# Performance work log

Measured on AMD Instinct MI355X. Metric: run time of the kernel, lower is better.

## Reference

```python
import jax, jax.numpy as jnp
import numpy as np


def setup_inputs() -> dict:
    key = jax.random.key(0)
    k1, k2, k3 = jax.random.split(key, 3)
    # q: [num_seqs, num_heads, head_dim] decode queries (q_len = 1)
    q = jax.random.normal(k1, (32, 32, 128), dtype=jnp.float32)
    # k, v: [sp_shards, num_seqs, kv_len_per_shard, num_kv_heads, head_dim]
    k = jax.random.normal(k2, (4, 32, 1024, 8, 128), dtype=jnp.float32)
    v = jax.random.normal(k3, (4, 32, 1024, 8, 128), dtype=jnp.float32)
    return {"q": q, "k": k, "v": v}


def reference(q, k, v):
    # Flash-decoding style paged decode attention with GQA:
    # each sequence-parallel shard s produces a partial (normalized) output
    # plus per-(seq, head) max logit and exp-sum; gatherlayer then performs
    # the online-softmax merge across shards.
    n, h, d = q.shape
    s, _, L, kv, _ = k.shape
    g = h // kv  # GQA group size
    scale = jnp.asarray(d, q.dtype) ** -0.5
    q4 = q.reshape(n, kv, g, d)

    # --- per-shard partial attention (what self.attn returns per rank) ---
    scores = jnp.einsum('nkgd,snlkd->snkgl', q4, k) * scale  # [s,n,kv,g,L]
    max_logits = scores.max(axis=-1)                          # [s,n,kv,g]
    p = jnp.exp(scores - max_logits[..., None])
    exp_sum = p.sum(axis=-1)                                  # [s,n,kv,g]
    partial = jnp.einsum('snkgl,snlkd->snkgd', p, v) / exp_sum[..., None]

    # --- gatherlayer: online-softmax combine across shards ---
    gmax = max_logits.max(axis=0)                             # [n,kv,g]
    w = jnp.exp(max_logits - gmax) * exp_sum                  # [s,n,kv,g]
    out = (partial * w[..., None]).sum(axis=0) / w.sum(axis=0)[..., None]
    return out.reshape(n, h, d)
```

## Files before the change

kernel.cpp:

```cpp
#include <hip/hip_runtime.h>
#include <math.h>

#define NSEQ 32
#define NH   32
#define NKV  8
#define GRP  4
#define DIM  128
#define NSH  4
#define LSH  1024
#define ITERS 128
#define KVSTRIDE (NKV*DIM)

#define MOFF ((size_t)NSH*NSEQ*NKV*GRP*DIM)
#define SOFF (MOFF + (size_t)NSH*NSEQ*NKV*GRP)

__global__ __launch_bounds__(256, 4) void attn_partial_kernel(
    const float* __restrict__ q, const float* __restrict__ kk,
    const float* __restrict__ vv, float* __restrict__ ws) {
  const int kvh = blockIdx.x;
  const int n   = blockIdx.y;
  const int sh  = blockIdx.z;
  const int tid = threadIdx.x;
  const int w    = tid >> 6;
  const int lane = tid & 63;
  const int sub  = lane & 31;
  const int pgrp = (w << 1) | (lane >> 5);

  const float scale = 0.08838834764831845f;
  const float* qp = q + ((size_t)n * NH + (size_t)kvh * GRP) * DIM + sub * 4;
  float4 qv0 = *(const float4*)(qp + 0 * DIM);
  float4 qv1 = *(const float4*)(qp + 1 * DIM);
  float4 qv2 = *(const float4*)(qp + 2 * DIM);
  float4 qv3 = *(const float4*)(qp + 3 * DIM);
#define SCQ(Q) Q.x *= scale; Q.y *= scale; Q.z *= scale; Q.w *= scale
  SCQ(qv0); SCQ(qv1); SCQ(qv2); SCQ(qv3);
#undef SCQ

  float m0 = -1e30f, m1 = -1e30f, m2 = -1e30f, m3 = -1e30f;
  float s0 = 0.f, s1 = 0.f, s2 = 0.f, s3 = 0.f;
  float4 a0 = make_float4(0.f,0.f,0.f,0.f);
  float4 a1 = a0, a2 = a0, a3 = a0;

  const size_t blkoff = ((size_t)sh * NSEQ + n) * LSH * (size_t)KVSTRIDE
                        + (size_t)kvh * DIM + sub * 4;
  const float* kb = kk + blkoff;
  const float* vb = vv + blkoff;

  auto process = [&](const float4 kc, const float4 vc) {
    float d0 = kc.x*qv0.x + kc.y*qv0.y + kc.z*qv0.z + kc.w*qv0.w;
    float d1 = kc.x*qv1.x + kc.y*qv1.y + kc.z*qv1.z + kc.w*qv1.w;
    float d2 = kc.x*qv2.x + kc.y*qv2.y + kc.z*qv2.z + kc.w*qv2.w;
    float d3 = kc.x*qv3.x + kc.y*qv3.y + kc.z*qv3.z + kc.w*qv3.w;
#pragma unroll
    for (int off = 1; off < 32; off <<= 1) {
      d0 += __shfl_xor(d0, off, 32);
      d1 += __shfl_xor(d1, off, 32);
      d2 += __shfl_xor(d2, off, 32);
      d3 += __shfl_xor(d3, off, 32);
    }
    if (d0 > m0 || d1 > m1 || d2 > m2 || d3 > m3) {
      float nm0 = fmaxf(m0, d0), nm1 = fmaxf(m1, d1);
      float nm2 = fmaxf(m2, d2), nm3 = fmaxf(m3, d3);
      float r0 = __expf(m0 - nm0), r1 = __expf(m1 - nm1);
      float r2 = __expf(m2 - nm2), r3 = __expf(m3 - nm3);
      s0 *= r0; s1 *= r1; s2 *= r2; s3 *= r3;
      a0.x *= r0; a0.y *= r0; a0.z *= r0; a0.w *= r0;
      a1.x *= r1; a1.y *= r1; a1.z *= r1; a1.w *= r1;
      a2.x *= r2; a2.y *= r2; a2.z *= r2; a2.w *= r2;
      a3.x *= r3; a3.y *= r3; a3.z *= r3; a3.w *= r3;
      m0 = nm0; m1 = nm1; m2 = nm2; m3 = nm3;
    }
    float p0 = __expf(d0 - m0), p1 = __expf(d1 - m1);
    float p2 = __expf(d2 - m2), p3 = __expf(d3 - m3);
    s0 += p0; s1 += p1; s2 += p2; s3 += p3;
    a0.x = fmaf(p0, vc.x, a0.x); a0.y = fmaf(p0, vc.y, a0.y);
    a0.z = fmaf(p0, vc.z, a0.z); a0.w = fmaf(p0, vc.w, a0.w);
    a1.x = fmaf(p1, vc.x, a1.x); a1.y = fmaf(p1, vc.y, a1.y);
    a1.z = fmaf(p1, vc.z, a1.z); a1.w = fmaf(p1, vc.w, a1.w);
    a2.x = fmaf(p2, vc.x, a2.x); a2.y = fmaf(p2, vc.y, a2.y);
    a2.z = fmaf(p2, vc.z, a2.z); a2.w = fmaf(p2, vc.w, a2.w);
    a3.x = fmaf(p3, vc.x, a3.x); a3.y = fmaf(p3, vc.y, a3.y);
    a3.z = fmaf(p3, vc.z, a3.z); a3.w = fmaf(p3, vc.w, a3.w);
  };

  float4 k0 = *(const float4*)(kb + (size_t)(0 * 8 + pgrp) * KVSTRIDE);
  float4 v0 = *(const float4*)(vb + (size_t)(0 * 8 + pgrp) * KVSTRIDE);
  float4 k1 = *(const float4*)(kb + (size_t)(1 * 8 + pgrp) * KVSTRIDE);
  float4 v1 = *(const float4*)(vb + (size_t)(1 * 8 + pgrp) * KVSTRIDE);

  for (int it = 0; it < ITERS - 2; it += 2) {
    const int p2i = it + 2;
    const int p3i = it + 3;
    float4 nk0 = *(const float4*)(kb + (size_t)(p2i * 8 + pgrp) * KVSTRIDE);
    float4 nv0 = *(const float4*)(vb + (size_t)(p2i * 8 + pgrp) * KVSTRIDE);
    float4 nk1 = *(const float4*)(kb + (size_t)(p3i * 8 + pgrp) * KVSTRIDE);
    float4 nv1 = *(const float4*)(vb + (size_t)(p3i * 8 + pgrp) * KVSTRIDE);
    process(k0, v0);
    process(k1, v1);
    k0 = nk0; v0 = nv0; k1 = nk1; v1 = nv1;
  }
  process(k0, v0);
  process(k1, v1);

#define HALF_MERGE(mX, sX, aX) do {                       \
    float om_ = __shfl_xor(mX, 32, 64);                   \
    float nm_ = fmaxf(mX, om_);                           \
    float ea_ = __expf(mX - nm_), eb_ = __expf(om_ - nm_);\
    float os_ = __shfl_xor(sX, 32, 64);                   \
    sX = sX * ea_ + os_ * eb_;                            \
    float t_;                                             \
    t_ = __shfl_xor(aX.x, 32, 64); aX.x = aX.x*ea_ + t_*eb_; \
    t_ = __shfl_xor(aX.y, 32, 64); aX.y = aX.y*ea_ + t_*eb_; \
    t_ = __shfl_xor(aX.z, 32, 64); aX.z = aX.z*ea_ + t_*eb_; \
    t_ = __shfl_xor(aX.w, 32, 64); aX.w = aX.w*ea_ + t_*eb_; \
    mX = nm_;                                             \
  } while (0)
  HALF_MERGE(m0, s0, a0);
  HALF_MERGE(m1, s1, a1);
  HALF_MERGE(m2, s2, a2);
  HALF_MERGE(m3, s3, a3);
#undef HALF_MERGE

  __shared__ float lm[4][GRP][32];
  __shared__ float lsum[4][GRP][32];
  __shared__ float la[4][GRP][32][4];
  if ((lane >> 5) == 0) {
#define STORE_G(gi, mX, sX, aX)                                   \
    lm[w][gi][sub] = mX; lsum[w][gi][sub] = sX;                   \
    la[w][gi][sub][0] = aX.x; la[w][gi][sub][1] = aX.y;           \
    la[w][gi][sub][2] = aX.z; la[w][gi][sub][3] = aX.w;
    STORE_G(0, m0, s0, a0)
    STORE_G(1, m1, s1, a1)
    STORE_G(2, m2, s2, a2)
    STORE_G(3, m3, s3, a3)
#undef STORE_G
  }
  __syncthreads();

  if (tid < 128) {
    const int gi = tid >> 5;
    const int sb = tid & 31;
    float M = -1e30f, SS = 0.f;
    float A0 = 0.f, A1 = 0.f, A2 = 0.f, A3 = 0.f;
#pragma unroll
    for (int wv = 0; wv < 4; ++wv) {
      float mm = lm[wv][gi][sb];
      float nm = fmaxf(M, mm);
      float ra = __expf(M - nm), rb = __expf(mm - nm);
      SS = SS * ra + lsum[wv][gi][sb] * rb;
      A0 = A0 * ra + la[wv][gi][sb][0] * rb;
      A1 = A1 * ra + la[wv][gi][sb][1] * rb;
      A2 = A2 * ra + la[wv][gi][sb][2] * rb;
      A3 = A3 * ra + la[wv][gi][sb][3] * rb;
      M = nm;
    }
    const size_t idx = (((size_t)sh * NSEQ + n) * NKV + kvh) * GRP + gi;
    *(float4*)(ws + idx * DIM + sb * 4) = make_float4(A0, A1, A2, A3);
    ws[MOFF + idx] = M;
    ws[SOFF + idx] = SS;
  }
}

__global__ __launch_bounds__(128) void attn_merge_kernel(
    const float* __restrict__ ws, float* __restrict__ out) {
  const int kvh = blockIdx.x;
  const int n   = blockIdx.y;
  const int d   = threadIdx.x;
#pragma unroll
  for (int gi = 0; gi < GRP; ++gi) {
    size_t idx[NSH];
    float mm[NSH];
    float M = -1e30f;
#pragma unroll
    for (int s2 = 0; s2 < NSH; ++s2) {
      idx[s2] = (((size_t)s2 * NSEQ + n) * NKV + kvh) * GRP + gi;
      mm[s2] = ws[MOFF + idx[s2]];
      M = fmaxf(M, mm[s2]);
    }
    float num = 0.f, den = 0.f;
#pragma unroll
    for (int s2 = 0; s2 < NSH; ++s2) {
      float wg = __expf(mm[s2] - M);
      den += wg * ws[SOFF + idx[s2]];
      num += wg * ws[idx[s2] * DIM + d];
    }
    out[((size_t)n * NH + (size_t)kvh * GRP + gi) * DIM + d] = num / den;
  }
}

extern "C" void kernel_launch(void* const* d_in, const int* in_sizes, int n_in,
                              void* d_out, int out_size, void* d_ws, size_t ws_size,
                              hipStream_t stream) {
  const float* q = (const float*)d_in[0];
  const float* k = (const float*)d_in[1];
  const float* v = (const float*)d_in[2];
  float* out = (float*)d_out;
  float* ws  = (float*)d_ws;

  attn_partial_kernel<<<dim3(NKV, NSEQ, NSH), 256, 0, stream>>>(q, k, v, ws);
  attn_merge_kernel<<<dim3(NKV, NSEQ), 128, 0, stream>>>(ws, out);
}
```

Baseline: 189.8 us.

## Split KV into row chunks with one half-wave per KV head

Adds a partial kernel in which each block covers a 128-row chunk of one shard across all 8 KV heads. Each half-wave handles one KV head, so a block reads whole contiguous KV rows instead of one strided 512-byte head slice per row. The block no longer merges across waves; each half-wave writes its own partial, giving 32 partials per (seq, head) that a larger merge kernel combines. This costs more workspace traffic and more merge work, and the new path is chosen only when the workspace is big enough, otherwise the old kernels run.

```diff
diff --git a/kernel.cpp b/kernel.cpp
--- a/kernel.cpp
+++ b/kernel.cpp
@@ -8,26 +8,33 @@
 #define DIM  128
 #define NSH  4
 #define LSH  1024
-#define ITERS 128
 #define KVSTRIDE (NKV*DIM)
+#define CHUNK 128
+#define NCHUNK (LSH/CHUNK)
+#define NPART (NSH*NCHUNK)
+
+#define MOFF2 ((size_t)NPART*NSEQ*NKV*GRP*DIM)
+#define SOFF2 (MOFF2 + (size_t)NPART*NSEQ*NKV*GRP)
+#define WS2_FLOATS (SOFF2 + (size_t)NPART*NSEQ*NKV*GRP)
 
 #define MOFF ((size_t)NSH*NSEQ*NKV*GRP*DIM)
 #define SOFF (MOFF + (size_t)NSH*NSEQ*NKV*GRP)
 
-__global__ __launch_bounds__(256, 4) void attn_partial_kernel(
+
+__global__ __launch_bounds__(256, 4) void attn_partial_rows(
     const float* __restrict__ q, const float* __restrict__ kk,
     const float* __restrict__ vv, float* __restrict__ ws) {
-  const int kvh = blockIdx.x;
+  const int c   = blockIdx.x;
   const int n   = blockIdx.y;
   const int sh  = blockIdx.z;
   const int tid = threadIdx.x;
   const int w    = tid >> 6;
   const int lane = tid & 63;
   const int sub  = lane & 31;
-  const int pgrp = (w << 1) | (lane >> 5);
+  const int hw   = (w << 1) | (lane >> 5);
 
   const float scale = 0.08838834764831845f;
-  const float* qp = q + ((size_t)n * NH + (size_t)kvh * GRP) * DIM + sub * 4;
+  const float* qp = q + ((size_t)n * NH + (size_t)hw * GRP) * DIM + sub * 4;
   float4 qv0 = *(const float4*)(qp + 0 * DIM);
   float4 qv1 = *(const float4*)(qp + 1 * DIM);
   float4 qv2 = *(const float4*)(qp + 2 * DIM);
@@ -41,8 +48,8 @@
   float4 a0 = make_float4(0.f,0.f,0.f,0.f);
   float4 a1 = a0, a2 = a0, a3 = a0;
 
-  const size_t blkoff = ((size_t)sh * NSEQ + n) * LSH * (size_t)KVSTRIDE
-                        + (size_t)kvh * DIM + sub * 4;
+  const size_t blkoff = (((size_t)sh * NSEQ + n) * LSH + (size_t)c * CHUNK)
+                        * (size_t)KVSTRIDE + (size_t)hw * DIM + sub * 4;
   const float* kb = kk + blkoff;
   const float* vb = vv + blkoff;
 
@@ -83,14 +90,141 @@
     a3.z = fmaf(p3, vc.z, a3.z); a3.w = fmaf(p3, vc.w, a3.w);
   };
 
+  float4 k0 = *(const float4*)(kb + (size_t)0 * KVSTRIDE);
+  float4 v0 = *(const float4*)(vb + (size_t)0 * KVSTRIDE);
+  float4 k1 = *(const float4*)(kb + (size_t)1 * KVSTRIDE);
+  float4 v1 = *(const float4*)(vb + (size_t)1 * KVSTRIDE);
+
+  for (int it = 0; it < CHUNK; it += 2) {
+    const int p2i = (it + 2) & (CHUNK - 1);
+    const int p3i = (it + 3) & (CHUNK - 1);
+    float4 nk0 = *(const float4*)(kb + (size_t)p2i * KVSTRIDE);
+    float4 nv0 = *(const float4*)(vb + (size_t)p2i * KVSTRIDE);
+    float4 nk1 = *(const float4*)(kb + (size_t)p3i * KVSTRIDE);
+    float4 nv1 = *(const float4*)(vb + (size_t)p3i * KVSTRIDE);
+    process(k0, v0);
+    process(k1, v1);
+    k0 = nk0; v0 = nv0; k1 = nk1; v1 = nv1;
+  }
+
+  const int part = sh * NCHUNK + c;
+  const size_t idx_base = (((size_t)part * NSEQ + n) * NKV + hw) * GRP;
+  *(float4*)(ws + (idx_base + 0) * DIM + sub * 4) = a0;
+  *(float4*)(ws + (idx_base + 1) * DIM + sub * 4) = a1;
+  *(float4*)(ws + (idx_base + 2) * DIM + sub * 4) = a2;
+  *(float4*)(ws + (idx_base + 3) * DIM + sub * 4) = a3;
+  if (sub < 4) {
+    float mv = (sub == 0) ? m0 : (sub == 1) ? m1 : (sub == 2) ? m2 : m3;
+    float sv = (sub == 0) ? s0 : (sub == 1) ? s1 : (sub == 2) ? s2 : s3;
+    ws[MOFF2 + idx_base + sub] = mv;
+    ws[SOFF2 + idx_base + sub] = sv;
+  }
+}
+
+__global__ __launch_bounds__(128) void attn_merge32(
+    const float* __restrict__ ws, float* __restrict__ out) {
+  const int kvh = blockIdx.x;
+  const int n   = blockIdx.y;
+  const int d   = threadIdx.x;
+#pragma unroll
+  for (int gi = 0; gi < GRP; ++gi) {
+    float mm[NPART];
+    float M = -1e30f;
+#pragma unroll
+    for (int p = 0; p < NPART; ++p) {
+      const size_t idx = (((size_t)p * NSEQ + n) * NKV + kvh) * GRP + gi;
+      mm[p] = ws[MOFF2 + idx];
+      M = fmaxf(M, mm[p]);
+    }
+    float num = 0.f, den = 0.f;
+#pragma unroll
+    for (int p = 0; p < NPART; ++p) {
+      const size_t idx = (((size_t)p * NSEQ + n) * NKV + kvh) * GRP + gi;
+      float wg = __expf(mm[p] - M);
+      den += wg * ws[SOFF2 + idx];
+      num += wg * ws[idx * DIM + d];
+    }
+    out[((size_t)n * NH + (size_t)kvh * GRP + gi) * DIM + d] = num / den;
+  }
+}
+
+__global__ __launch_bounds__(256, 4) void attn_partial_kernel(
+    const float* __restrict__ q, const float* __restrict__ kk,
+    const float* __restrict__ vv, float* __restrict__ ws) {
+  const int kvh = blockIdx.x;
+  const int n   = blockIdx.y;
+  const int sh  = blockIdx.z;
+  const int tid = threadIdx.x;
+  const int w    = tid >> 6;
+  const int lane = tid & 63;
+  const int sub  = lane & 31;
+  const int pgrp = (w << 1) | (lane >> 5);
+
+  const float scale = 0.08838834764831845f;
+  const float* qp = q + ((size_t)n * NH + (size_t)kvh * GRP) * DIM + sub * 4;
+  float4 qv0 = *(const float4*)(qp + 0 * DIM);
+  float4 qv1 = *(const float4*)(qp + 1 * DIM);
+  float4 qv2 = *(const float4*)(qp + 2 * DIM);
+  float4 qv3 = *(const float4*)(qp + 3 * DIM);
+#define SCQ(Q) Q.x *= scale; Q.y *= scale; Q.z *= scale; Q.w *= scale
+  SCQ(qv0); SCQ(qv1); SCQ(qv2); SCQ(qv3);
+#undef SCQ
+
+  float m0 = -1e30f, m1 = -1e30f, m2 = -1e30f, m3 = -1e30f;
+  float s0 = 0.f, s1 = 0.f, s2 = 0.f, s3 = 0.f;
+  float4 a0 = make_float4(0.f,0.f,0.f,0.f);
+  float4 a1 = a0, a2 = a0, a3 = a0;
+
+  const size_t blkoff = ((size_t)sh * NSEQ + n) * LSH * (size_t)KVSTRIDE
+                        + (size_t)kvh * DIM + sub * 4;
+  const float* kb = kk + blkoff;
+  const float* vb = vv + blkoff;
+
+  auto process = [&](const float4 kc, const float4 vc) {
+    float d0 = kc.x*qv0.x + kc.y*qv0.y + kc.z*qv0.z + kc.w*qv0.w;
+    float d1 = kc.x*qv1.x + kc.y*qv1.y + kc.z*qv1.z + kc.w*qv1.w;
+    float d2 = kc.x*qv2.x + kc.y*qv2.y + kc.z*qv2.z + kc.w*qv2.w;
+    float d3 = kc.x*qv3.x + kc.y*qv3.y + kc.z*qv3.z + kc.w*qv3.w;
+#pragma unroll
+    for (int off = 1; off < 32; off <<= 1) {
+      d0 += __shfl_xor(d0, off, 32);
+      d1 += __shfl_xor(d1, off, 32);
+      d2 += __shfl_xor(d2, off, 32);
+      d3 += __shfl_xor(d3, off, 32);
+    }
+    if (d0 > m0 || d1 > m1 || d2 > m2 || d3 > m3) {
+      float nm0 = fmaxf(m0, d0), nm1 = fmaxf(m1, d1);
+      float nm2 = fmaxf(m2, d2), nm3 = fmaxf(m3, d3);
+      float r0 = __expf(m0 - nm0), r1 = __expf(m1 - nm1);
+      float r2 = __expf(m2 - nm2), r3 = __expf(m3 - nm3);
+      s0 *= r0; s1 *= r1; s2 *= r2; s3 *= r3;
+      a0.x *= r0; a0.y *= r0; a0.z *= r0; a0.w *= r0;
+      a1.x *= r1; a1.y *= r1; a1.z *= r1; a1.w *= r1;
+      a2.x *= r2; a2.y *= r2; a2.z *= r2; a2.w *= r2;
+      a3.x *= r3; a3.y *= r3; a3.z *= r3; a3.w *= r3;
+      m0 = nm0; m1 = nm1; m2 = nm2; m3 = nm3;
+    }
+    float p0 = __expf(d0 - m0), p1 = __expf(d1 - m1);
+    float p2 = __expf(d2 - m2), p3 = __expf(d3 - m3);
+    s0 += p0; s1 += p1; s2 += p2; s3 += p3;
+    a0.x = fmaf(p0, vc.x, a0.x); a0.y = fmaf(p0, vc.y, a0.y);
+    a0.z = fmaf(p0, vc.z, a0.z); a0.w = fmaf(p0, vc.w, a0.w);
+    a1.x = fmaf(p1, vc.x, a1.x); a1.y = fmaf(p1, vc.y, a1.y);
+    a1.z = fmaf(p1, vc.z, a1.z); a1.w = fmaf(p1, vc.w, a1.w);
+    a2.x = fmaf(p2, vc.x, a2.x); a2.y = fmaf(p2, vc.y, a2.y);
+    a2.z = fmaf(p2, vc.z, a2.z); a2.w = fmaf(p2, vc.w, a2.w);
+    a3.x = fmaf(p3, vc.x, a3.x); a3.y = fmaf(p3, vc.y, a3.y);
+    a3.z = fmaf(p3, vc.z, a3.z); a3.w = fmaf(p3, vc.w, a3.w);
+  };
+
   float4 k0 = *(const float4*)(kb + (size_t)(0 * 8 + pgrp) * KVSTRIDE);
   float4 v0 = *(const float4*)(vb + (size_t)(0 * 8 + pgrp) * KVSTRIDE);
   float4 k1 = *(const float4*)(kb + (size_t)(1 * 8 + pgrp) * KVSTRIDE);
   float4 v1 = *(const float4*)(vb + (size_t)(1 * 8 + pgrp) * KVSTRIDE);
 
-  for (int it = 0; it < ITERS - 2; it += 2) {
-    const int p2i = it + 2;
-    const int p3i = it + 3;
+  for (int it = 0; it < 128; it += 2) {
+    const int p2i = (it + 2) & 127;
+    const int p3i = (it + 3) & 127;
     float4 nk0 = *(const float4*)(kb + (size_t)(p2i * 8 + pgrp) * KVSTRIDE);
     float4 nv0 = *(const float4*)(vb + (size_t)(p2i * 8 + pgrp) * KVSTRIDE);
     float4 nk1 = *(const float4*)(kb + (size_t)(p3i * 8 + pgrp) * KVSTRIDE);
@@ -99,8 +233,6 @@
     process(k1, v1);
     k0 = nk0; v0 = nv0; k1 = nk1; v1 = nv1;
   }
-  process(k0, v0);
-  process(k1, v1);
 
 #define HALF_MERGE(mX, sX, aX) do {                       \
     float om_ = __shfl_xor(mX, 32, 64);                   \
@@ -197,6 +329,11 @@
   float* out = (float*)d_out;
   float* ws  = (float*)d_ws;
 
-  attn_partial_kernel<<<dim3(NKV, NSEQ, NSH), 256, 0, stream>>>(q, k, v, ws);
-  attn_merge_kernel<<<dim3(NKV, NSEQ), 128, 0, stream>>>(ws, out);
-}
+  if (ws_size >= WS2_FLOATS * sizeof(float)) {
+    attn_partial_rows<<<dim3(NCHUNK, NSEQ, NSH), 256, 0, stream>>>(q, k, v, ws);
+    attn_merge32<<<dim3(NKV, NSEQ), 128, 0, stream>>>(ws, out);
+  } else {
+    attn_partial_kernel<<<dim3(NKV, NSEQ, NSH), 256, 0, stream>>>(q, k, v, ws);
+    attn_merge_kernel<<<dim3(NKV, NSEQ), 128, 0, stream>>>(ws, out);
+  }
+}
```

New measurement: 222.8 us. 1.17x slower.
